# Kernel optimization log

Hardware: AMD Instinct MI355X
Metric: run time of the kernel (lower is better)

Reference implementation:

```python
import jax, jax.numpy as jnp
import numpy as np

C = 64   # in_channels
KS = 3   # kernel_size


def _wconv(p, W1, b1, W2, b2, W3, b3):
    # 1x1 conv stack: 3 -> 64 -> 256 -> C*KS*KS, ReLU between
    h = jax.nn.relu(jnp.einsum('oc,bchw->bohw', W1, p) + b1[None, :, None, None])
    h = jax.nn.relu(jnp.einsum('oc,bchw->bohw', W2, h) + b2[None, :, None, None])
    h = jnp.einsum('oc,bchw->bohw', W3, h) + b3[None, :, None, None]
    return h  # [1, C*KS*KS, ho, wo]


def setup_inputs() -> dict:
    key = jax.random.key(0)
    k = jax.random.split(key, 8)
    bs, hi, wi = 2, 128, 128
    ho, wo = 512, 512
    x = jax.random.normal(k[0], (bs, C, hi, wi), jnp.float32)
    poseMap = jax.random.normal(k[1], (1, 3, ho, wo), jnp.float32)
    interMapY = jax.random.randint(k[2], (ho, wo), 0, hi)
    interMapX = jax.random.randint(k[3], (ho, wo), 0, wi)
    W1 = jax.random.normal(k[4], (64, 3), jnp.float32) * 0.1
    b1 = jnp.zeros((64,), jnp.float32)
    W2 = jax.random.normal(k[5], (256, 64), jnp.float32) * 0.05
    b2 = jnp.zeros((256,), jnp.float32)
    W3 = jax.random.normal(k[6], (C * KS * KS, 256), jnp.float32) * 0.05
    b3 = jnp.zeros((C * KS * KS,), jnp.float32)
    return {'x': x, 'poseMap': poseMap, 'W1': W1, 'b1': b1, 'W2': W2, 'b2': b2,
            'W3': W3, 'b3': b3, 'interMapY': interMapY, 'interMapX': interMapX}


def reference(x, poseMap, W1, b1, W2, b2, W3, b3, interMapY, interMapX):
    bs, c, hi, wi = x.shape
    ho, wo = interMapY.shape
    # kernel prediction branch (poseMap is detached in the original)
    w = _wconv(jax.lax.stop_gradient(poseMap), W1, b1, W2, b2, W3, b3)
    w = w.reshape(C, KS * KS, ho, wo)
    sw = jax.nn.softmax(w, axis=1)  # softmax over the KS*KS taps
    # unfold(x, KS, padding=KS//2) tap k corresponds to xp[:, :, i + k//KS, j + k%KS]
    pad = KS // 2
    xp = jnp.pad(x, ((0, 0), (0, 0), (pad, pad), (pad, pad)))
    out = jnp.zeros((bs, C, ho, wo), x.dtype)
    for k in range(KS * KS):  # fixed small loop over taps; fuses gather+weight+reduce
        dy, dx = k // KS, k % KS
        g = xp[:, :, interMapY + dy, interMapX + dx]  # [bs, C, ho, wo] paired gather
        out = out + g * sw[None, :, k]  # sw[:, k] -> [C, ho, wo]
    return out
```

## Files before the change

kernel.cpp:

```cpp
#include <hip/hip_runtime.h>
#include <math.h>

#define HO 512
#define WO 512
#define HI 128
#define WI 128
#define CC 64
#define BS 2
#define NPX 64
#define NT 256

#define W2P_ELEMS (16 * 2 * 64 * 8)
#define W3P_ELEMS (36 * 8 * 64 * 8)
#define XT_ELEM_OFF (W2P_ELEMS + W3P_ELEMS)
#define XT_FLOATS (130 * 130 * 128)

typedef __attribute__((ext_vector_type(8))) short short8;
typedef __attribute__((ext_vector_type(4))) float float4v;
typedef __attribute__((ext_vector_type(2))) float float2v;

__device__ __forceinline__ unsigned short f2bf(float f) {
    unsigned u = __builtin_bit_cast(unsigned, f);
    unsigned r = (u + 0x7FFFu + ((u >> 16) & 1u)) >> 16;
    return (unsigned short)r;
}

__global__ void prepack_zw(const float* __restrict__ W2,
                           const float* __restrict__ W3,
                           unsigned short* __restrict__ wsp,
                           float* __restrict__ xt) {
    const int total = W2P_ELEMS + W3P_ELEMS;
    for (int idx = blockIdx.x * blockDim.x + threadIdx.x; idx < total;
         idx += gridDim.x * blockDim.x) {
        float v;
        if (idx < W2P_ELEMS) {
            int j = idx & 7, lane = (idx >> 3) & 63, rest = idx >> 9;
            int ks = rest & 1, nt = rest >> 1;
            int n = nt * 16 + (lane & 15);
            int k = ks * 32 + (lane >> 4) * 8 + j;
            v = W2[n * 64 + k];
        } else {
            int i2 = idx - W2P_ELEMS;
            int j = i2 & 7, lane = (i2 >> 3) & 63, rest = i2 >> 9;
            int ks = rest & 7, nt = rest >> 3;
            int tap = nt >> 2, ct = nt & 3;
            int row = (ct * 16 + (lane & 15)) * 9 + tap;
            int k = ks * 32 + (lane >> 4) * 8 + j;
            v = W3[row * 256 + k];
        }
        wsp[idx] = f2bf(v);
    }
    float4v z = {0.f, 0.f, 0.f, 0.f};
    float4v* xt4 = (float4v*)xt;
    for (int i = blockIdx.x * blockDim.x + threadIdx.x; i < XT_FLOATS / 4;
         i += gridDim.x * blockDim.x)
        xt4[i] = z;
}

__global__ void prepack_x(const float* __restrict__ x, float* __restrict__ xt) {
    const int tid = blockIdx.x * blockDim.x + threadIdx.x;
    const int pos = tid & 16383;
    const int g   = tid >> 14;
    const int h = pos >> 7, w = pos & 127;
    const float* src = x + pos;
    float a0[4], a1[4];
    #pragma unroll
    for (int j = 0; j < 4; ++j) a0[j] = src[(size_t)(g * 4 + j) * (HI * WI)];
    #pragma unroll
    for (int j = 0; j < 4; ++j) a1[j] = src[(size_t)(CC + g * 4 + j) * (HI * WI)];
    float* dst = xt + ((h + 1) * 130 + (w + 1)) * 128 + g * 8;
    *(float4v*)dst       = (float4v){a0[0], a1[0], a0[1], a1[1]};
    *(float4v*)(dst + 4) = (float4v){a0[2], a1[2], a0[3], a1[3]};
}

__global__ __launch_bounds__(NT, 3)
void fused_main(const float* __restrict__ xt, const float* __restrict__ pose,
                const float* __restrict__ W1, const float* __restrict__ b1,
                const float* __restrict__ b2, const float* __restrict__ b3,
                const int* __restrict__ iY, const int* __restrict__ iX,
                const unsigned short* __restrict__ wsp,
                float* __restrict__ out)
{
    __shared__ char smem[33792 + 17408 + 768 + 512];
    unsigned short (*sH2)[264] = (unsigned short (*)[264])&smem[0];
    unsigned short (*sH1)[72]  = (unsigned short (*)[72])&smem[33792];
    float (*sOut)[2][16][68]   = (float (*)[2][16][68])&smem[33792];
    float (*sP)[NPX]           = (float (*)[NPX])&smem[51200];
    int* sIY                   = (int*)&smem[51968];
    int* sIX                   = (int*)&smem[52224];

    const int t = threadIdx.x;
    const int pixBase = blockIdx.x * NPX;
    const int y  = pixBase / WO;
    const int x0 = pixBase % WO;

    if (t < 192) sP[t >> 6][t & 63] = pose[(t >> 6) * (HO * WO) + pixBase + (t & 63)];
    if (t < 64) sIY[t] = iY[pixBase + t];
    else if (t < 128) sIX[t - 64] = iX[pixBase + t - 64];
    __syncthreads();

    {
        const int p  = t & 63;
        const int og = t >> 6;
        const float p0 = sP[0][p], p1 = sP[1][p], p2 = sP[2][p];
        #pragma unroll
        for (int i = 0; i < 16; i += 2) {
            const int o = og * 16 + i;
            float a0 = fmaf(W1[o * 3 + 2], p2, fmaf(W1[o * 3 + 1], p1, fmaf(W1[o * 3 + 0], p0, b1[o])));
            float a1 = fmaf(W1[o * 3 + 5], p2, fmaf(W1[o * 3 + 4], p1, fmaf(W1[o * 3 + 3], p0, b1[o + 1])));
            a0 = fmaxf(a0, 0.f); a1 = fmaxf(a1, 0.f);
            unsigned pack = (unsigned)f2bf(a0) | ((unsigned)f2bf(a1) << 16);
            *(unsigned*)&sH1[p][o] = pack;
        }
    }
    __syncthreads();

    const int wv = t >> 6, l = t & 63, lm = l & 15, lq = l >> 4;
    const int m0 = wv * 16;

    {
        short8 a0 = *(const short8*)&sH1[m0 + lm][0  + lq * 8];
        short8 a1 = *(const short8*)&sH1[m0 + lm][32 + lq * 8];
        const short8* w2f = (const short8*)wsp;
        #pragma unroll 4
        for (int nt = 0; nt < 16; ++nt) {
            float4v acc = {0.f, 0.f, 0.f, 0.f};
            short8 bf0 = w2f[(nt * 2 + 0) * 64 + l];
            short8 bf1 = w2f[(nt * 2 + 1) * 64 + l];
            acc = __builtin_amdgcn_mfma_f32_16x16x32_bf16(a0, bf0, acc, 0, 0, 0);
            acc = __builtin_amdgcn_mfma_f32_16x16x32_bf16(a1, bf1, acc, 0, 0, 0);
            const float bv = b2[nt * 16 + lm];
            #pragma unroll
            for (int r = 0; r < 4; ++r)
                sH2[m0 + lq * 4 + r][nt * 16 + lm] = f2bf(fmaxf(acc[r] + bv, 0.f));
        }
    }
    __syncthreads();

    int pbase[4];
    #pragma unroll
    for (int r = 0; r < 4; ++r) {
        const int p = m0 + lq * 4 + r;
        pbase[r] = ((sIY[p] + 1) * 130 + (sIX[p] + 1)) * 128;
    }
    const int koff[9] = {-131 * 128, -130 * 128, -129 * 128,
                         -1 * 128,   0,          1 * 128,
                         129 * 128,  130 * 128,  131 * 128};
    const short8* w3f = (const short8*)(wsp + W2P_ELEMS);

    for (int ct = 0; ct < 4; ++ct) {
        float4v accs[9];
        #pragma unroll
        for (int tap = 0; tap < 9; ++tap) accs[tap] = (float4v){0.f, 0.f, 0.f, 0.f};

        #pragma unroll 2
        for (int ks = 0; ks < 8; ++ks) {
            short8 a = *(const short8*)&sH2[m0 + lm][ks * 32 + lq * 8];
            #pragma unroll
            for (int tap = 0; tap < 9; ++tap) {
                short8 b = w3f[(((tap << 2) | ct) * 8 + ks) * 64 + l];
                accs[tap] = __builtin_amdgcn_mfma_f32_16x16x32_bf16(a, b, accs[tap], 0, 0, 0);
            }
        }

        const int c = ct * 16 + lm;
        float bv[9];
        #pragma unroll
        for (int tap = 0; tap < 9; ++tap) bv[tap] = b3[c * 9 + tap];

        float ob0[4], ob1[4];
        #pragma unroll
        for (int r = 0; r < 4; ++r) {
            float lg[9];
            #pragma unroll
            for (int tap = 0; tap < 9; ++tap) lg[tap] = accs[tap][r] + bv[tap];
            float mx = lg[0];
            #pragma unroll
            for (int tap = 1; tap < 9; ++tap) mx = fmaxf(mx, lg[tap]);
            const float* xb = xt + pbase[r] + 2 * c;
            float s = 0.f, o0 = 0.f, o1 = 0.f;
            #pragma unroll
            for (int tap = 0; tap < 9; ++tap) {
                const float ev = __expf(lg[tap] - mx);
                const float2v gg = *(const float2v*)(xb + koff[tap]);
                s += ev;
                o0 = fmaf(ev, gg[0], o0);
                o1 = fmaf(ev, gg[1], o1);
            }
            const float inv = 1.f / s;
            ob0[r] = o0 * inv;
            ob1[r] = o1 * inv;
        }

        float (*so)[16][68] = sOut[ct & 1];
        *(float4v*)&so[0][lm][m0 + lq * 4] = (float4v){ob0[0], ob0[1], ob0[2], ob0[3]};
        *(float4v*)&so[1][lm][m0 + lq * 4] = (float4v){ob1[0], ob1[1], ob1[2], ob1[3]};
        __syncthreads();

        const int row = t >> 3;
        const int b   = row >> 4, ch = row & 15;
        const int seg = (t & 7) * 8;
        float4v v0 = *(float4v*)&so[b][ch][seg];
        float4v v1 = *(float4v*)&so[b][ch][seg + 4];
        float* op = out + (((size_t)(b * CC + ct * 16 + ch) * HO) + y) * WO + x0 + seg;
        *(float4v*)op = v0;
        *(float4v*)(op + 4) = v1;
    }
}

extern "C" void kernel_launch(void* const* d_in, const int* in_sizes, int n_in,
                              void* d_out, int out_size, void* d_ws, size_t ws_size,
                              hipStream_t stream) {
    const float* x    = (const float*)d_in[0];
    const float* pose = (const float*)d_in[1];
    const float* W1   = (const float*)d_in[2];
    const float* b1   = (const float*)d_in[3];
    const float* W2   = (const float*)d_in[4];
    const float* b2   = (const float*)d_in[5];
    const float* W3   = (const float*)d_in[6];
    const float* b3   = (const float*)d_in[7];
    const int*   iY   = (const int*)d_in[8];
    const int*   iX   = (const int*)d_in[9];
    float* out = (float*)d_out;
    unsigned short* wsp = (unsigned short*)d_ws;
    float* xt = (float*)((char*)d_ws + XT_ELEM_OFF * sizeof(unsigned short));

    prepack_zw<<<2048, NT, 0, stream>>>(W2, W3, wsp, xt);
    prepack_x<<<1024, NT, 0, stream>>>(x, xt);

    const int nblocks = (HO * WO) / NPX;
    fused_main<<<nblocks, NT, 0, stream>>>(
        xt, pose, W1, b1, b2, b3, iY, iX, wsp, out);
}
```

Before: 395.6 us.

## Merge prepack kernels, zero only halo border, vectorize layer-2 LDS stores

Folds the weight prepack and the x transpose into one launch. The full-buffer zeroing of the padded x tensor is replaced by writes to the one-cell halo border only, which removes a multi-megabyte memory clear and one kernel launch. In the layer-2 MFMA the A and B operands are swapped so the accumulators are transposed, letting each lane load its bias as a float4 and write packed short4 rows into shared memory. It also processes two output tiles per iteration. The risk is the more complex border index arithmetic, and possible LDS bank conflicts from the new store pattern.

```diff
diff --git a/kernel.cpp b/kernel.cpp
--- a/kernel.cpp
+++ b/kernel.cpp
@@ -12,10 +12,12 @@
 
 #define W2P_ELEMS (16 * 2 * 64 * 8)
 #define W3P_ELEMS (36 * 8 * 64 * 8)
-#define XT_ELEM_OFF (W2P_ELEMS + W3P_ELEMS)
-#define XT_FLOATS (130 * 130 * 128)
+#define TOTALW    (W2P_ELEMS + W3P_ELEMS)
+#define XT_ELEM_OFF TOTALW
+#define NBORDER4  16512
 
 typedef __attribute__((ext_vector_type(8))) short short8;
+typedef __attribute__((ext_vector_type(4))) short short4v;
 typedef __attribute__((ext_vector_type(4))) float float4v;
 typedef __attribute__((ext_vector_type(2))) float float2v;
 
@@ -25,52 +27,60 @@
     return (unsigned short)r;
 }
 
-__global__ void prepack_zw(const float* __restrict__ W2,
-                           const float* __restrict__ W3,
-                           unsigned short* __restrict__ wsp,
-                           float* __restrict__ xt) {
-    const int total = W2P_ELEMS + W3P_ELEMS;
-    for (int idx = blockIdx.x * blockDim.x + threadIdx.x; idx < total;
-         idx += gridDim.x * blockDim.x) {
-        float v;
-        if (idx < W2P_ELEMS) {
-            int j = idx & 7, lane = (idx >> 3) & 63, rest = idx >> 9;
-            int ks = rest & 1, nt = rest >> 1;
-            int n = nt * 16 + (lane & 15);
-            int k = ks * 32 + (lane >> 4) * 8 + j;
-            v = W2[n * 64 + k];
+__global__ void prepack_all(const float* __restrict__ x,
+                            const float* __restrict__ W2,
+                            const float* __restrict__ W3,
+                            unsigned short* __restrict__ wsp,
+                            float* __restrict__ xt) {
+    const int tid = blockIdx.x * blockDim.x + threadIdx.x;
+    if (tid < 262144) {
+        const int pos = tid & 16383;
+        const int g   = tid >> 14;
+        const int h = pos >> 7, w = pos & 127;
+        const float* src = x + pos;
+        float a0[4], a1[4];
+        #pragma unroll
+        for (int j = 0; j < 4; ++j) a0[j] = src[(size_t)(g * 4 + j) * (HI * WI)];
+        #pragma unroll
+        for (int j = 0; j < 4; ++j) a1[j] = src[(size_t)(CC + g * 4 + j) * (HI * WI)];
+        float* dst = xt + ((h + 1) * 130 + (w + 1)) * 128 + g * 8;
+        *(float4v*)dst       = (float4v){a0[0], a1[0], a0[1], a1[1]};
+        *(float4v*)(dst + 4) = (float4v){a0[2], a1[2], a0[3], a1[3]};
+        return;
+    }
+    const int idx = tid - 262144;
+    if (idx < W2P_ELEMS) {
+        int j = idx & 7, lane = (idx >> 3) & 63, rest = idx >> 9;
+        int ks = rest & 1, nt = rest >> 1;
+        int n = nt * 16 + (lane & 15);
+        int k = ks * 32 + (lane >> 4) * 8 + j;
+        wsp[idx] = f2bf(W2[n * 64 + k]);
+    } else if (idx < TOTALW) {
+        int i2 = idx - W2P_ELEMS;
+        int j = i2 & 7, lane = (i2 >> 3) & 63, rest = i2 >> 9;
+        int ks = rest & 7, nt = rest >> 3;
+        int tap = nt >> 2, ct = nt & 3;
+        int row = (ct * 16 + (lane & 15)) * 9 + tap;
+        int k = ks * 32 + (lane >> 4) * 8 + j;
+        wsp[idx] = f2bf(W3[row * 256 + k]);
+    } else if (idx < TOTALW + NBORDER4) {
+        int a = idx - TOTALW;
+        int cell;
+        if (a < 2 * 130 * 32) {
+            int r = a / (130 * 32);
+            int rest = a - r * (130 * 32);
+            cell = (r * 129) * 130 + (rest >> 5);
+            a = rest;
         } else {
-            int i2 = idx - W2P_ELEMS;
-            int j = i2 & 7, lane = (i2 >> 3) & 63, rest = i2 >> 9;
-            int ks = rest & 7, nt = rest >> 3;
-            int tap = nt >> 2, ct = nt & 3;
-            int row = (ct * 16 + (lane & 15)) * 9 + tap;
-            int k = ks * 32 + (lane >> 4) * 8 + j;
-            v = W3[row * 256 + k];
-        }
-        wsp[idx] = f2bf(v);
-    }
-    float4v z = {0.f, 0.f, 0.f, 0.f};
-    float4v* xt4 = (float4v*)xt;
-    for (int i = blockIdx.x * blockDim.x + threadIdx.x; i < XT_FLOATS / 4;
-         i += gridDim.x * blockDim.x)
-        xt4[i] = z;
-}
-
-__global__ void prepack_x(const float* __restrict__ x, float* __restrict__ xt) {
-    const int tid = blockIdx.x * blockDim.x + threadIdx.x;
-    const int pos = tid & 16383;
-    const int g   = tid >> 14;
-    const int h = pos >> 7, w = pos & 127;
-    const float* src = x + pos;
-    float a0[4], a1[4];
-    #pragma unroll
-    for (int j = 0; j < 4; ++j) a0[j] = src[(size_t)(g * 4 + j) * (HI * WI)];
-    #pragma unroll
-    for (int j = 0; j < 4; ++j) a1[j] = src[(size_t)(CC + g * 4 + j) * (HI * WI)];
-    float* dst = xt + ((h + 1) * 130 + (w + 1)) * 128 + g * 8;
-    *(float4v*)dst       = (float4v){a0[0], a1[0], a0[1], a1[1]};
-    *(float4v*)(dst + 4) = (float4v){a0[2], a1[2], a0[3], a1[3]};
+            int a2 = a - 2 * 130 * 32;
+            int h = 1 + (a2 >> 6);
+            int rest = a2 & 63;
+            cell = h * 130 + (rest >> 5) * 129;
+            a = rest;
+        }
+        float4v z = {0.f, 0.f, 0.f, 0.f};
+        *(float4v*)(xt + (size_t)cell * 128 + (a & 31) * 4) = z;
+    }
 }
 
 __global__ __launch_bounds__(NT, 3)
@@ -123,16 +133,27 @@
         short8 a1 = *(const short8*)&sH1[m0 + lm][32 + lq * 8];
         const short8* w2f = (const short8*)wsp;
         #pragma unroll 4
-        for (int nt = 0; nt < 16; ++nt) {
-            float4v acc = {0.f, 0.f, 0.f, 0.f};
-            short8 bf0 = w2f[(nt * 2 + 0) * 64 + l];
-            short8 bf1 = w2f[(nt * 2 + 1) * 64 + l];
-            acc = __builtin_amdgcn_mfma_f32_16x16x32_bf16(a0, bf0, acc, 0, 0, 0);
-            acc = __builtin_amdgcn_mfma_f32_16x16x32_bf16(a1, bf1, acc, 0, 0, 0);
-            const float bv = b2[nt * 16 + lm];
-            #pragma unroll
-            for (int r = 0; r < 4; ++r)
-                sH2[m0 + lq * 4 + r][nt * 16 + lm] = f2bf(fmaxf(acc[r] + bv, 0.f));
+        for (int kc = 0; kc < 8; ++kc) {
+            const int ntE = 2 * kc, ntO = 2 * kc + 1;
+            float4v aE = {0.f, 0.f, 0.f, 0.f}, aO = {0.f, 0.f, 0.f, 0.f};
+            short8 e0 = w2f[(ntE * 2 + 0) * 64 + l];
+            short8 e1 = w2f[(ntE * 2 + 1) * 64 + l];
+            short8 o0 = w2f[(ntO * 2 + 0) * 64 + l];
+            short8 o1 = w2f[(ntO * 2 + 1) * 64 + l];
+            aE = __builtin_amdgcn_mfma_f32_16x16x32_bf16(e0, a0, aE, 0, 0, 0);
+            aE = __builtin_amdgcn_mfma_f32_16x16x32_bf16(e1, a1, aE, 0, 0, 0);
+            aO = __builtin_amdgcn_mfma_f32_16x16x32_bf16(o0, a0, aO, 0, 0, 0);
+            aO = __builtin_amdgcn_mfma_f32_16x16x32_bf16(o1, a1, aO, 0, 0, 0);
+            const float4v bE = *(const float4v*)(b2 + ntE * 16 + lq * 4);
+            const float4v bO = *(const float4v*)(b2 + ntO * 16 + lq * 4);
+            short4v hE, hO;
+            #pragma unroll
+            for (int r = 0; r < 4; ++r) {
+                hE[r] = (short)f2bf(fmaxf(aE[r] + bE[r], 0.f));
+                hO[r] = (short)f2bf(fmaxf(aO[r] + bO[r], 0.f));
+            }
+            *(short4v*)&sH2[m0 + lm][kc * 32 + lq * 4]      = hE;
+            *(short4v*)&sH2[m0 + lm][kc * 32 + 16 + lq * 4] = hO;
         }
     }
     __syncthreads();
@@ -223,10 +244,9 @@
     const int*   iX   = (const int*)d_in[9];
     float* out = (float*)d_out;
     unsigned short* wsp = (unsigned short*)d_ws;
-    float* xt = (float*)((char*)d_ws + XT_ELEM_OFF * sizeof(unsigned short));
-
-    prepack_zw<<<2048, NT, 0, stream>>>(W2, W3, wsp, xt);
-    prepack_x<<<1024, NT, 0, stream>>>(x, xt);
+    float* xt = (float*)((char*)d_ws + (size_t)XT_ELEM_OFF * sizeof(unsigned short));
+
+    prepack_all<<<2048, NT, 0, stream>>>(x, W2, W3, wsp, xt);
 
     const int nblocks = (HO * WO) / NPX;
     fused_main<<<nblocks, NT, 0, stream>>>(
```

Result: no change. 399.5 us (+1.0%).
